# Kernel optimization log

Measured on AMD Instinct MI355X. Metric: run time of the kernel, lower is better.

Reference implementation:

```python
import jax, jax.numpy as jnp
import numpy as np

B, T, H, D = 16, 128, 512, 256
VIN, VOUT = 32000, 32000


def _lstm_cell(xt, h, c, W, U, b):
    # Keras LSTMCell gate order: i, f, g(candidate), o
    z = xt @ W + h @ U + b  # [B, 4H]
    i, f, g, o = jnp.split(z, 4, axis=-1)
    c = jax.nn.sigmoid(f) * c + jax.nn.sigmoid(i) * jnp.tanh(g)
    h = jax.nn.sigmoid(o) * jnp.tanh(c)
    return h, c


def _lstm_seq(x, W, U, b, h0, c0):
    # x: [B,T,Din] -> seq [B,T,H], final (h,c)
    def step(carry, xt):
        h, c = _lstm_cell(xt, carry[0], carry[1], W, U, b)
        return (h, c), h
    (hT, cT), seq = jax.lax.scan(step, (h0, c0), jnp.swapaxes(x, 0, 1))
    return jnp.swapaxes(seq, 0, 1), hT, cT


def setup_inputs() -> dict:
    key = jax.random.key(0)
    ks = jax.random.split(key, 16)
    s = lambda fan: 1.0 / np.sqrt(fan).astype(np.float32)
    f32 = jnp.float32
    return {
        "tokens": jax.random.randint(ks[0], (B, T), 0, VIN + 1),
        "emb": jax.random.normal(ks[1], (VIN + 1, D), f32) * 0.02,
        "W1": jax.random.normal(ks[2], (D, 4 * H), f32) * s(D),
        "U1": jax.random.normal(ks[3], (H, 4 * H), f32) * s(H),
        "b1": jnp.zeros((4 * H,), f32),
        "W2": jax.random.normal(ks[4], (H, 4 * H), f32) * s(H),
        "U2": jax.random.normal(ks[5], (H, 4 * H), f32) * s(H),
        "b2": jnp.zeros((4 * H,), f32),
        "Wd1": jax.random.normal(ks[6], (H, 4 * H), f32) * s(H),
        "Ud1": jax.random.normal(ks[7], (H, 4 * H), f32) * s(H),
        "bd1": jnp.zeros((4 * H,), f32),
        "Wd2": jax.random.normal(ks[8], (H, 4 * H), f32) * s(H),
        "Ud2": jax.random.normal(ks[9], (H, 4 * H), f32) * s(H),
        "bd2": jnp.zeros((4 * H,), f32),
        "Wo": jax.random.normal(ks[10], (2 * H, VOUT + 1), f32) * s(2 * H),
        "bo": jnp.zeros((VOUT + 1,), f32),
    }


def reference(tokens, emb, W1, U1, b1, W2, U2, b2, Wd1, Ud1, bd1, Wd2, Ud2, bd2, Wo, bo):
    x = emb[tokens]  # [B,T,D]
    zeros = jnp.zeros((tokens.shape[0], H), x.dtype)
    seq1, h1, c1 = _lstm_seq(x, W1, U1, b1, zeros, zeros)
    # layer-2 encoder initialized with layer-1 final states (as in source)
    seq2, h2, c2 = _lstm_seq(seq1, W2, U2, b2, h1, c1)

    def dec_step(carry, xt):
        (hA, cA), (hB, cB) = carry
        hA, cA = _lstm_cell(xt, hA, cA, Wd1, Ud1, bd1)
        hB, cB = _lstm_cell(hA, hB, cB, Wd2, Ud2, bd2)
        # global Luong dot attention over full encoder-2 sequence
        score = jax.nn.softmax(jnp.einsum('bsh,bh->bs', seq2, hB), axis=-1)
        ctx = jnp.einsum('bsh,bs->bh', seq2, score)
        out = jnp.concatenate([hB, ctx], axis=-1)  # [B, 2H]
        return ((hA, cA), (hB, cB)), out

    # decoder input is the encoder-2 sequence, time-major
    _, outs = jax.lax.scan(dec_step, ((h1, c1), (h2, c2)), jnp.swapaxes(seq2, 0, 1))
    dec = jnp.swapaxes(outs, 0, 1)  # [B,T,2H]
    logits = dec @ Wo + bo  # [B,T,VOUT+1]
    return jax.nn.softmax(logits, axis=-1)
```

## Files before the change

### kernel.cpp

```cpp
#include <hip/hip_runtime.h>
#include <hip/hip_bf16.h>
#include <math.h>

#define Bq   16
#define Tq   128
#define Hq   512
#define Dq   256
#define G4H  2048
#define MR   2048
#define VO   32001
#define NPAD 32128
#define BH   (Bq * Hq)
#define SENTW 0x7FC0u
#define SENT64 0x7FC07FC07FC07FC0ull
#define NANW 0x7FC00000u
#define SPINCAP (1 << 20)

typedef unsigned int u32;
typedef unsigned long long u64;
typedef __attribute__((ext_vector_type(4))) float f32x4;
typedef __attribute__((ext_vector_type(8))) short bfrag;
typedef __attribute__((ext_vector_type(4))) float facc;

__device__ __forceinline__ float bf2f(short s) {
  union { unsigned u; float f; } v; v.u = ((unsigned)(unsigned short)s) << 16; return v.f;
}
__device__ __forceinline__ short f2bf(float f) {
  union { float f; unsigned u; } v; v.f = f;
  unsigned r = (v.u + 0x7fffu + ((v.u >> 16) & 1u)) >> 16;
  return (short)r;
}
__device__ __forceinline__ float asf(u32 u) {
  union { u32 u; float f; } v; v.u = u; return v.f;
}
__device__ __forceinline__ u32 fbits(float f) {
  union { float f; u32 u; } v; v.f = f; return v.u;
}
__device__ __forceinline__ float sigm(float x) { return 1.0f / (1.0f + expf(-x)); }

__device__ __forceinline__ void ic_store64(u64* p, u64 v) {
  __hip_atomic_store(p, v, __ATOMIC_RELAXED, __HIP_MEMORY_SCOPE_AGENT);
}
__device__ __forceinline__ u64 ic_load64(const u64* p) {
  return __hip_atomic_load(p, __ATOMIC_RELAXED, __HIP_MEMORY_SCOPE_AGENT);
}
__device__ __forceinline__ void ic_store32(u32* p, u32 v) {
  __hip_atomic_store(p, v, __ATOMIC_RELAXED, __HIP_MEMORY_SCOPE_AGENT);
}
__device__ __forceinline__ u32 ic_load32(const u32* p) {
  return __hip_atomic_load(p, __ATOMIC_RELAXED, __HIP_MEMORY_SCOPE_AGENT);
}

__device__ __forceinline__ void* swz(void* plane, int row, int byteoff) {
  return (void*)((char*)plane + row * 1040 + (byteoff ^ ((row & 7) << 4)));
}

__device__ __forceinline__ void stage_h(void* p0, void* p1, const u64 v[8]) {
  #pragma unroll
  for (int it = 0; it < 8; ++it) {
    int i = it * 512 + threadIdx.x;
    int b = i >> 8, bo = (i & 255) * 4;
    *(u32*)swz(p0, b, bo) = (u32)v[it];
    *(u32*)swz(p1, b, bo) = (u32)(v[it] >> 32);
  }
}
__device__ __forceinline__ void stage_x(void* p0, const u32 w[8]) {
  #pragma unroll
  for (int it = 0; it < 8; ++it) {
    int i = it * 512 + threadIdx.x;
    int b = i >> 8, bo = (i & 255) * 4;
    *(u32*)swz(p0, b, bo) = w[it];
  }
}

__global__ __launch_bounds__(256) void k_fill(u64* __restrict__ p, int n) {
  int i = blockIdx.x * 256 + threadIdx.x;
  if (i < n) p[i] = SENT64;
}
__global__ __launch_bounds__(256) void k_fillf(u32* __restrict__ p, int n) {
  int i = blockIdx.x * 256 + threadIdx.x;
  if (i < n) p[i] = NANW;
}

__global__ __launch_bounds__(256) void k_transcvt(const float* __restrict__ in,
                                                  short* __restrict__ out,
                                                  int R, int N, int perm) {
  __shared__ float tile[32][33];
  int nb = blockIdx.x * 32, rb = blockIdx.y * 32;
  int tx = threadIdx.x & 31, ty = threadIdx.x >> 5;
  for (int i = 0; i < 4; ++i) {
    int r = rb + ty + i * 8;
    int n = nb + tx;
    tile[ty + i * 8][tx] = (n < N) ? in[(size_t)r * N + n] : 0.0f;
  }
  __syncthreads();
  for (int i = 0; i < 4; ++i) {
    int n = nb + ty + i * 8;
    int orow = perm ? (((n & 511) << 2) | (n >> 9)) : n;
    out[(size_t)orow * R + rb + tx] = f2bf(tile[tx][ty + i * 8]);
  }
}

__global__ __launch_bounds__(256) void k_gather(const int* __restrict__ tokens,
                                                const float* __restrict__ emb,
                                                short* __restrict__ xbf) {
  int row = blockIdx.x;
  int t = row >> 4, b = row & 15;
  int tok = tokens[b * Tq + t];
  xbf[(size_t)row * Dq + threadIdx.x] = f2bf(emb[(size_t)tok * Dq + threadIdx.x]);
}

__global__ __launch_bounds__(256) void k_gemm(const short* __restrict__ A,
                                              const short* __restrict__ BT,
                                              float* __restrict__ C,
                                              const float* __restrict__ bias,
                                              int M, int Nreal, int K, int ldc,
                                              int permb) {
  __shared__ short lA[128 * 64];
  __shared__ short lB[128 * 64];
  const int tid = threadIdx.x;
  const int wave = tid >> 6, lane = tid & 63;
  const int l15 = lane & 15, l4 = lane >> 4;
  const int m0 = blockIdx.y * 128, n0 = blockIdx.x * 128;
  const int wm = (wave >> 1) * 64, wn = (wave & 1) * 64;
  facc acc[4][4] = {};

  for (int k0 = 0; k0 < K; k0 += 64) {
    __syncthreads();
    for (int i = 0; i < 4; ++i) {
      int c = i * 256 + wave * 64 + lane;
      int r = c >> 3, q = c & 7;
      int qs = q ^ (r & 7);
      const short* ga = A + (size_t)(m0 + r) * K + k0 + qs * 8;
      const short* gb = BT + (size_t)(n0 + r) * K + k0 + qs * 8;
      short* la = lA + (size_t)(i * 256 + wave * 64) * 8;
      short* lb = lB + (size_t)(i * 256 + wave * 64) * 8;
      __builtin_amdgcn_global_load_lds((const __attribute__((address_space(1))) u32*)ga,
                                       (__attribute__((address_space(3))) u32*)la, 16, 0, 0);
      __builtin_amdgcn_global_load_lds((const __attribute__((address_space(1))) u32*)gb,
                                       (__attribute__((address_space(3))) u32*)lb, 16, 0, 0);
    }
    __syncthreads();
    for (int ks = 0; ks < 2; ++ks) {
      bfrag a[4], b[4];
      for (int mi = 0; mi < 4; ++mi) {
        int r = wm + mi * 16 + l15;
        int qs = (ks * 4 + l4) ^ (r & 7);
        a[mi] = *(const bfrag*)&lA[r * 64 + qs * 8];
      }
      for (int ni = 0; ni < 4; ++ni) {
        int r = wn + ni * 16 + l15;
        int qs = (ks * 4 + l4) ^ (r & 7);
        b[ni] = *(const bfrag*)&lB[r * 64 + qs * 8];
      }
      for (int mi = 0; mi < 4; ++mi)
        for (int ni = 0; ni < 4; ++ni)
          acc[mi][ni] = __builtin_amdgcn_mfma_f32_16x16x32_bf16(a[mi], b[ni], acc[mi][ni], 0, 0, 0);
    }
  }
  for (int ni = 0; ni < 4; ++ni) {
    int col = n0 + wn + ni * 16 + l15;
    if (col >= Nreal) continue;
    int bcol = permb ? (((col & 3) << 9) | (col >> 2)) : col;
    float bs = bias ? bias[bcol] : 0.0f;
    for (int mi = 0; mi < 4; ++mi) {
      int rb = m0 + wm + mi * 16 + l4 * 4;
      facc v = acc[mi][ni];
      C[(size_t)(rb + 0) * ldc + col] = v[0] + bs;
      C[(size_t)(rb + 1) * ldc + col] = v[1] + bs;
      C[(size_t)(rb + 2) * ldc + col] = v[2] + bs;
      C[(size_t)(rb + 3) * ldc + col] = v[3] + bs;
    }
  }
}

__global__ __launch_bounds__(512, 1) void k_mega(
    const float* __restrict__ XW,
    const short* __restrict__ U1T, const short* __restrict__ U2T,
    const short* __restrict__ W2T, const short* __restrict__ Ud1T,
    const short* __restrict__ Wd1T, const short* __restrict__ Ud2T,
    const short* __restrict__ Wd2T,
    const float* __restrict__ b2, const float* __restrict__ bd1,
    const float* __restrict__ bd2,
    u64* __restrict__ h1buf, u64* __restrict__ h2buf,
    u64* __restrict__ hAbuf, u64* __restrict__ hBbuf,
    u32* __restrict__ xs1, u32* __restrict__ xs2,
    u32* __restrict__ h1f, u32* __restrict__ c1f,
    u32* __restrict__ h2f, u32* __restrict__ c2f,
    short* __restrict__ seq2_bf, short* __restrict__ hBseq_bf,
    short* __restrict__ dec_bf)
{
  __shared__ short pl[4][16][520];
  __shared__ float zt[8][16][20];
  const int grp  = blockIdx.x >> 5;
  const int rank = blockIdx.x & 31;
  const int tid = threadIdx.x;
  const int wv = tid >> 6, lane = tid & 63;
  const int l15 = lane & 15, l4 = lane >> 4;
  const int kh = wv >> 2;
  const int gw = rank * 4 + (wv & 3);
  const int bb = lane >> 2, jj = lane & 3;
  const int hidx = gw * 4 + jj;
  const int idx = bb * Hq + hidx;
  const int pi = idx >> 1;

  const short* urs = (grp == 0) ? U1T : (grp == 1) ? U2T : (grp == 2) ? Ud1T : Ud2T;
  const short* wrs = (grp == 1) ? W2T : (grp == 2) ? Wd1T : (grp == 3) ? Wd2T : U1T;
  const float* bias = (grp == 1) ? b2 : (grp == 2) ? bd1 : bd2;
  u64* own = (grp == 0) ? h1buf : (grp == 1) ? h2buf : (grp == 2) ? hAbuf : hBbuf;
  const u32* xin = (grp == 1) ? xs1 : xs2;
  u32* xout = (grp == 0) ? xs1 : (grp == 1) ? xs2 : nullptr;

  bfrag ur[8], wr[8];
  {
    size_t ro = (size_t)(gw * 16 + l15) * Hq + kh * 256 + l4 * 8;
    #pragma unroll
    for (int ks = 0; ks < 8; ++ks) {
      ur[ks] = *(const bfrag*)&urs[ro + ks * 32];
      wr[ks] = *(const bfrag*)&wrs[ro + ks * 32];
    }
  }
  float bi = 0, bf_ = 0, bg_ = 0, bo_ = 0;
  if (grp != 0 && wv < 4) {
    bi = bias[hidx]; bf_ = bias[Hq + hidx];
    bg_ = bias[2 * Hq + hidx]; bo_ = bias[3 * Hq + hidx];
  }
  float c = 0.0f;
  if (wv < 4) {
    float hv = 0.0f;
    if (grp != 0) {
      const u32* hf = (grp == 3) ? h2f : h1f;
      const u32* cf = (grp == 3) ? c2f : c1f;
      u32 hw = NANW, cw = NANW;
      for (int spin = 0; spin < SPINCAP; ++spin) {
        hw = ic_load32(&hf[idx]); cw = ic_load32(&cf[idx]);
        if (hw != NANW && cw != NANW) break;
        __builtin_amdgcn_s_sleep(32);
      }
      hv = asf(hw); c = asf(cw);
    }
    int hi_ = (int)(unsigned short)f2bf(hv);
    int lo_ = (int)(unsigned short)f2bf(hv - bf2f((short)hi_));
    int hi2 = __shfl_xor(hi_, 1), lo2 = __shfl_xor(lo_, 1);
    if ((jj & 1) == 0) {
      u64 v = (u64)((u32)hi_ | ((u32)hi2 << 16)) | ((u64)((u32)lo_ | ((u32)lo2 << 16)) << 32);
      ic_store64(&own[pi], v);
    }
  }
  __syncthreads();

  for (int s = 0; s < Tq; ++s) {
    f32x4 xg = {};
    if (grp == 0 && wv < 4)
      xg = *(const f32x4*)&XW[(size_t)(s * Bq + bb) * G4H + hidx * 4];

    u64 v[8], vx[8];
    u32 w[8];
    const u64* ph = own + (size_t)s * 4096 + tid;
    if (grp == 0) {
      for (int spin = 0;; ++spin) {
        #pragma unroll
        for (int it = 0; it < 8; ++it) v[it] = ic_load64(&ph[it * 512]);
        u32 bad = 0;
        #pragma unroll
        for (int it = 0; it < 8; ++it) bad |= (((u32)v[it] & 0xFFFFu) == SENTW);
        if (!bad || spin >= SPINCAP) break;
        __builtin_amdgcn_s_sleep(1);
      }
    } else if (grp != 3) {
      const u32* px = xin + (size_t)s * 4096 + tid;
      for (int spin = 0;; ++spin) {
        #pragma unroll
        for (int it = 0; it < 8; ++it) v[it] = ic_load64(&ph[it * 512]);
        #pragma unroll
        for (int it = 0; it < 8; ++it) w[it] = ic_load32(&px[it * 512]);
        u32 bad = 0;
        #pragma unroll
        for (int it = 0; it < 8; ++it) {
          bad |= (((u32)v[it] & 0xFFFFu) == SENTW);
          bad |= ((w[it] & 0xFFFFu) == SENTW);
        }
        if (!bad || spin >= SPINCAP) break;
        __builtin_amdgcn_s_sleep(1);
      }
    } else {
      const u64* pa = hAbuf + (size_t)(s + 1) * 4096 + tid;
      for (int spin = 0;; ++spin) {
        #pragma unroll
        for (int it = 0; it < 8; ++it) v[it]  = ic_load64(&ph[it * 512]);
        #pragma unroll
        for (int it = 0; it < 8; ++it) vx[it] = ic_load64(&pa[it * 512]);
        u32 bad = 0;
        #pragma unroll
        for (int it = 0; it < 8; ++it) {
          bad |= (((u32)v[it]  & 0xFFFFu) == SENTW);
          bad |= (((u32)vx[it] & 0xFFFFu) == SENTW);
        }
        if (!bad || spin >= SPINCAP) break;
        __builtin_amdgcn_s_sleep(1);
      }
    }
    stage_h(&pl[0][0][0], &pl[1][0][0], v);
    if (grp == 1 || grp == 2) stage_x(&pl[2][0][0], w);
    else if (grp == 3)        stage_h(&pl[2][0][0], &pl[3][0][0], vx);
    __syncthreads();

    facc a0 = {}, a1 = {}, a2 = {}, a3 = {};
    #pragma unroll
    for (int ks = 0; ks < 8; ++ks) {
      int bo = kh * 512 + ks * 64 + l4 * 16;
      bfrag hh = *(const bfrag*)swz(&pl[0][0][0], l15, bo);
      bfrag hl = *(const bfrag*)swz(&pl[1][0][0], l15, bo);
      a0 = __builtin_amdgcn_mfma_f32_16x16x32_bf16(hh, ur[ks], a0, 0, 0, 0);
      a1 = __builtin_amdgcn_mfma_f32_16x16x32_bf16(hl, ur[ks], a1, 0, 0, 0);
      if (grp == 1 || grp == 2) {
        bfrag xh = *(const bfrag*)swz(&pl[2][0][0], l15, bo);
        a2 = __builtin_amdgcn_mfma_f32_16x16x32_bf16(xh, wr[ks], a2, 0, 0, 0);
      } else if (grp == 3) {
        bfrag xh = *(const bfrag*)swz(&pl[2][0][0], l15, bo);
        bfrag xl = *(const bfrag*)swz(&pl[3][0][0], l15, bo);
        a2 = __builtin_amdgcn_mfma_f32_16x16x32_bf16(xh, wr[ks], a2, 0, 0, 0);
        a3 = __builtin_amdgcn_mfma_f32_16x16x32_bf16(xl, wr[ks], a3, 0, 0, 0);
      }
    }
    a0 += a1;
    if (grp != 0) a0 += a2;
    if (grp == 3) a0 += a3;
    *(f32x4*)&zt[wv][l15][l4 * 4] = a0;
    __syncthreads();

    if (wv < 4) {
      float zi = zt[wv][4 * jj + 0][bb] + zt[wv + 4][4 * jj + 0][bb];
      float zf = zt[wv][4 * jj + 1][bb] + zt[wv + 4][4 * jj + 1][bb];
      float zg = zt[wv][4 * jj + 2][bb] + zt[wv + 4][4 * jj + 2][bb];
      float zo = zt[wv][4 * jj + 3][bb] + zt[wv + 4][4 * jj + 3][bb];
      if (grp == 0) { zi += xg[0]; zf += xg[1]; zg += xg[2]; zo += xg[3]; }
      else          { zi += bi;    zf += bf_;   zg += bg_;   zo += bo_;  }
      c = sigm(zf) * c + sigm(zi) * tanhf(zg);
      float hN = sigm(zo) * tanhf(c);
      int hi_ = (int)(unsigned short)f2bf(hN);
      int lo_ = (int)(unsigned short)f2bf(hN - bf2f((short)hi_));
      int hi2 = __shfl_xor(hi_, 1), lo2 = __shfl_xor(lo_, 1);
      if ((jj & 1) == 0) {
        u64 pv = (u64)((u32)hi_ | ((u32)hi2 << 16)) | ((u64)((u32)lo_ | ((u32)lo2 << 16)) << 32);
        ic_store64(&own[(size_t)(s + 1) * 4096 + pi], pv);
        if (xout) ic_store32(&xout[(size_t)s * 4096 + pi], (u32)pv);
      }
      if (grp == 1) seq2_bf[(size_t)(s * Bq + bb) * Hq + hidx] = (short)hi_;
      if (grp == 3) {
        hBseq_bf[(size_t)(s * Bq + bb) * Hq + hidx] = (short)hi_;
        dec_bf[((size_t)bb * Tq + s) * (2 * Hq) + hidx] = (short)hi_;
      }
      if (s == Tq - 1) {
        if (grp == 0) { ic_store32(&h1f[idx], fbits(hN)); ic_store32(&c1f[idx], fbits(c)); }
        if (grp == 1) { ic_store32(&h2f[idx], fbits(hN)); ic_store32(&c2f[idx], fbits(c)); }
      }
    }
  }
}

__global__ __launch_bounds__(256) void k_attn(const short* __restrict__ seq2b,
                                              const short* __restrict__ hqb,
                                              short* __restrict__ decb) {
  int blk = blockIdx.x;
  int b = blk >> 7, t = blk & 127;
  __shared__ u32 q[256];
  __shared__ float part[256];
  __shared__ float p[Tq];
  int tid = threadIdx.x;
  q[tid] = *(const u32*)&hqb[(size_t)(t * Bq + b) * Hq + tid * 2];
  __syncthreads();
  {
    int s = tid >> 1, half = tid & 1;
    const u32* row = (const u32*)&seq2b[(size_t)(s * Bq + b) * Hq + half * 256];
    const u32* qh = q + half * 128;
    float a = 0.0f;
    #pragma unroll 8
    for (int k = 0; k < 128; ++k) {
      u32 r = row[k], qq = qh[k];
      a += asf(r << 16) * asf(qq << 16) + asf(r & 0xFFFF0000u) * asf(qq & 0xFFFF0000u);
    }
    part[tid] = a;
  }
  __syncthreads();
  if (tid < 64) {
    float v0 = part[2 * tid] + part[2 * tid + 1];
    float v1 = part[2 * (tid + 64)] + part[2 * (tid + 64) + 1];
    float mx = fmaxf(v0, v1);
    for (int off = 32; off; off >>= 1) mx = fmaxf(mx, __shfl_xor(mx, off));
    float e0 = __expf(v0 - mx), e1 = __expf(v1 - mx);
    float sm = e0 + e1;
    for (int off = 32; off; off >>= 1) sm += __shfl_xor(sm, off);
    float inv = 1.0f / sm;
    p[tid] = e0 * inv; p[tid + 64] = e1 * inv;
  }
  __syncthreads();
  float c0 = 0.0f, c1 = 0.0f;
  for (int s = 0; s < Tq; ++s) {
    float ps = p[s];
    u32 r = *(const u32*)&seq2b[(size_t)(s * Bq + b) * Hq + tid * 2];
    c0 += ps * asf(r << 16);
    c1 += ps * asf(r & 0xFFFF0000u);
  }
  u32 o = ((u32)(unsigned short)f2bf(c0)) | (((u32)(unsigned short)f2bf(c1)) << 16);
  *(u32*)&decb[(size_t)(b * Tq + t) * (2 * Hq) + Hq + tid * 2] = o;
}

__global__ __launch_bounds__(256) void k_softmax(float* __restrict__ L) {
  int row = blockIdx.x;
  float* p = L + (size_t)row * VO;
  int tid = threadIdx.x;
  float m = -3.0e38f, s = 0.0f;
  for (int i = tid; i < VO; i += 256) {
    float v = p[i];
    float mn = fmaxf(m, v);
    s = s * __expf(m - mn) + __expf(v - mn);
    m = mn;
  }
  __shared__ float sm[256], ss[256];
  sm[tid] = m; ss[tid] = s;
  __syncthreads();
  for (int off = 128; off; off >>= 1) {
    if (tid < off) {
      float m2 = sm[tid + off], s2 = ss[tid + off];
      float mn = fmaxf(sm[tid], m2);
      ss[tid] = ss[tid] * __expf(sm[tid] - mn) + s2 * __expf(m2 - mn);
      sm[tid] = mn;
    }
    __syncthreads();
  }
  float M = sm[0], IS = 1.0f / ss[0];
  for (int i = tid; i < VO; i += 256) {
    p[i] = __expf(p[i] - M) * IS;
  }
}

extern "C" void kernel_launch(void* const* d_in, const int* in_sizes, int n_in,
                              void* d_out, int out_size, void* d_ws, size_t ws_size,
                              hipStream_t stream) {
  const int*   tokens = (const int*)d_in[0];
  const float* emb    = (const float*)d_in[1];
  const float* W1     = (const float*)d_in[2];
  const float* U1     = (const float*)d_in[3];
  const float* b1     = (const float*)d_in[4];
  const float* W2     = (const float*)d_in[5];
  const float* U2     = (const float*)d_in[6];
  const float* b2     = (const float*)d_in[7];
  const float* Wd1    = (const float*)d_in[8];
  const float* Ud1    = (const float*)d_in[9];
  const float* bd1    = (const float*)d_in[10];
  const float* Wd2    = (const float*)d_in[11];
  const float* Ud2    = (const float*)d_in[12];
  const float* bd2    = (const float*)d_in[13];
  const float* Wo     = (const float*)d_in[14];
  const float* bo     = (const float*)d_in[15];
  float* out = (float*)d_out;

  size_t off = 0;
  char* base = (char*)d_ws;
  auto alloc = [&](size_t bytes) -> void* {
    void* p = base + off;
    off += (bytes + 255) & ~(size_t)255;
    return p;
  };
  short* x_bf    = (short*)alloc((size_t)MR * Dq * 2);
  short* W1T     = (short*)alloc((size_t)G4H * Dq * 2);
  short* WoT     = (short*)alloc((size_t)NPAD * (2 * Hq) * 2);
  short* U1T     = (short*)alloc((size_t)G4H * Hq * 2);
  short* U2T     = (short*)alloc((size_t)G4H * Hq * 2);
  short* W2T     = (short*)alloc((size_t)G4H * Hq * 2);
  short* Ud1T    = (short*)alloc((size_t)G4H * Hq * 2);
  short* Wd1T    = (short*)alloc((size_t)G4H * Hq * 2);
  short* Ud2T    = (short*)alloc((size_t)G4H * Hq * 2);
  short* Wd2T    = (short*)alloc((size_t)G4H * Hq * 2);
  float* XW      = (float*)alloc((size_t)MR * G4H * 4);
  short* seq2_bf = (short*)alloc((size_t)MR * Hq * 2);
  short* hBseqbf = (short*)alloc((size_t)MR * Hq * 2);
  short* dec_bf  = (short*)alloc((size_t)MR * 2 * Hq * 2);
  u64*   hflow   = (u64*)alloc((size_t)516 * 4096 * 8);
  u32*   xs1     = (u32*)alloc((size_t)128 * 4096 * 4);
  u32*   xs2     = (u32*)alloc((size_t)128 * 4096 * 4);
  u32*   h1f     = (u32*)alloc(BH * 4);
  u32*   c1f     = (u32*)alloc(BH * 4);
  u32*   h2f     = (u32*)alloc(BH * 4);
  u32*   c2f     = (u32*)alloc(BH * 4);
  u64* h1buf = hflow;
  u64* h2buf = hflow + (size_t)129 * 4096;
  u64* hAbuf = hflow + (size_t)258 * 4096;
  u64* hBbuf = hflow + (size_t)387 * 4096;
  (void)ws_size; (void)in_sizes; (void)n_in; (void)out_size;

  {
    int n64 = 516 * 4096 + 2 * (128 * 4096 / 2);
    k_fill<<<(n64 + 255) / 256, 256, 0, stream>>>(hflow, n64);
    k_fillf<<<(4 * BH + 255) / 256, 256, 0, stream>>>(h1f, 4 * BH);
  }

  k_transcvt<<<dim3(G4H / 32, Dq / 32), 256, 0, stream>>>(W1, W1T, Dq, G4H, 1);
  k_transcvt<<<dim3(G4H / 32, Hq / 32), 256, 0, stream>>>(U1, U1T, Hq, G4H, 1);
  k_transcvt<<<dim3(G4H / 32, Hq / 32), 256, 0, stream>>>(U2, U2T, Hq, G4H, 1);
  k_transcvt<<<dim3(G4H / 32, Hq / 32), 256, 0, stream>>>(W2, W2T, Hq, G4H, 1);
  k_transcvt<<<dim3(G4H / 32, Hq / 32), 256, 0, stream>>>(Ud1, Ud1T, Hq, G4H, 1);
  k_transcvt<<<dim3(G4H / 32, Hq / 32), 256, 0, stream>>>(Wd1, Wd1T, Hq, G4H, 1);
  k_transcvt<<<dim3(G4H / 32, Hq / 32), 256, 0, stream>>>(Ud2, Ud2T, Hq, G4H, 1);
  k_transcvt<<<dim3(G4H / 32, Hq / 32), 256, 0, stream>>>(Wd2, Wd2T, Hq, G4H, 1);
  k_transcvt<<<dim3(NPAD / 32, (2 * Hq) / 32), 256, 0, stream>>>(Wo, WoT, 2 * Hq, VO, 0);

  k_gather<<<MR, 256, 0, stream>>>(tokens, emb, x_bf);

  k_gemm<<<dim3(G4H / 128, MR / 128), 256, 0, stream>>>(x_bf, W1T, XW, b1, MR, G4H, Dq, G4H, 1);

  k_mega<<<128, 512, 0, stream>>>(XW, U1T, U2T, W2T, Ud1T, Wd1T, Ud2T, Wd2T,
                                  b2, bd1, bd2,
                                  h1buf, h2buf, hAbuf, hBbuf, xs1, xs2,
                                  h1f, c1f, h2f, c2f,
                                  seq2_bf, hBseqbf, dec_bf);

  k_attn<<<MR, 256, 0, stream>>>(seq2_bf, hBseqbf, dec_bf);
  k_gemm<<<dim3(NPAD / 128, MR / 128), 256, 0, stream>>>(dec_bf, WoT, out, bo, MR, VO, 2 * Hq, VO, 0);
  k_softmax<<<MR, 256, 0, stream>>>(out);
}
```

Baseline: 2.411 ms.

## Split persistent LSTM megakernel into staged launches with hi/lo input precision

Replaces the single 128-block persistent kernel that ran all four LSTM layers as a wavefront pipeline with three sequential launches: encoder layer 1 alone, then encoder layer 2 together with decoder cell A, then decoder cell B. Final h/c states now cross launch boundaries through plain memory instead of NaN-sentinel spin polls, which removes the extra fill kernel and the bf16 x-stream buffers. Cell inputs are now staged as hi+lo bf16 pairs with two MFMAs, where before only the hi part was used for groups 1 and 2. The cost is the lost overlap between stages, so the four-layer critical path becomes roughly serial, and each step does more MFMA work.

Result: no change. 2.395 ms (-0.7%).

```diff
diff --git a/kernel.cpp b/kernel.cpp
--- a/kernel.cpp
+++ b/kernel.cpp
@@ -13,7 +13,6 @@
 #define BH   (Bq * Hq)
 #define SENTW 0x7FC0u
 #define SENT64 0x7FC07FC07FC07FC0ull
-#define NANW 0x7FC00000u
 #define SPINCAP (1 << 20)
 
 typedef unsigned int u32;
@@ -33,21 +32,12 @@
 __device__ __forceinline__ float asf(u32 u) {
   union { u32 u; float f; } v; v.u = u; return v.f;
 }
-__device__ __forceinline__ u32 fbits(float f) {
-  union { float f; u32 u; } v; v.f = f; return v.u;
-}
 __device__ __forceinline__ float sigm(float x) { return 1.0f / (1.0f + expf(-x)); }
 
 __device__ __forceinline__ void ic_store64(u64* p, u64 v) {
   __hip_atomic_store(p, v, __ATOMIC_RELAXED, __HIP_MEMORY_SCOPE_AGENT);
 }
 __device__ __forceinline__ u64 ic_load64(const u64* p) {
-  return __hip_atomic_load(p, __ATOMIC_RELAXED, __HIP_MEMORY_SCOPE_AGENT);
-}
-__device__ __forceinline__ void ic_store32(u32* p, u32 v) {
-  __hip_atomic_store(p, v, __ATOMIC_RELAXED, __HIP_MEMORY_SCOPE_AGENT);
-}
-__device__ __forceinline__ u32 ic_load32(const u32* p) {
   return __hip_atomic_load(p, __ATOMIC_RELAXED, __HIP_MEMORY_SCOPE_AGENT);
 }
 
@@ -64,22 +54,10 @@
     *(u32*)swz(p1, b, bo) = (u32)(v[it] >> 32);
   }
 }
-__device__ __forceinline__ void stage_x(void* p0, const u32 w[8]) {
-  #pragma unroll
-  for (int it = 0; it < 8; ++it) {
-    int i = it * 512 + threadIdx.x;
-    int b = i >> 8, bo = (i & 255) * 4;
-    *(u32*)swz(p0, b, bo) = w[it];
-  }
-}
 
 __global__ __launch_bounds__(256) void k_fill(u64* __restrict__ p, int n) {
   int i = blockIdx.x * 256 + threadIdx.x;
   if (i < n) p[i] = SENT64;
-}
-__global__ __launch_bounds__(256) void k_fillf(u32* __restrict__ p, int n) {
-  int i = blockIdx.x * 256 + threadIdx.x;
-  if (i < n) p[i] = NANW;
 }
 
 __global__ __launch_bounds__(256) void k_transcvt(const float* __restrict__ in,
@@ -174,26 +152,104 @@
   }
 }
 
-__global__ __launch_bounds__(512, 1) void k_mega(
-    const float* __restrict__ XW,
-    const short* __restrict__ U1T, const short* __restrict__ U2T,
-    const short* __restrict__ W2T, const short* __restrict__ Ud1T,
-    const short* __restrict__ Wd1T, const short* __restrict__ Ud2T,
-    const short* __restrict__ Wd2T,
-    const float* __restrict__ b2, const float* __restrict__ bd1,
-    const float* __restrict__ bd2,
-    u64* __restrict__ h1buf, u64* __restrict__ h2buf,
-    u64* __restrict__ hAbuf, u64* __restrict__ hBbuf,
-    u32* __restrict__ xs1, u32* __restrict__ xs2,
-    u32* __restrict__ h1f, u32* __restrict__ c1f,
-    u32* __restrict__ h2f, u32* __restrict__ c2f,
-    short* __restrict__ seq2_bf, short* __restrict__ hBseq_bf,
-    short* __restrict__ dec_bf)
-{
+
+__global__ __launch_bounds__(512, 1) void k_rec1(const float* __restrict__ XW,
+                                                 const short* __restrict__ UT,
+                                                 u64* __restrict__ hbuf,
+                                                 float* __restrict__ hfin,
+                                                 float* __restrict__ cfin) {
+  __shared__ short lh[2][16][520];
+  __shared__ float zt[8][16][20];
+  const int tid = threadIdx.x;
+  const int wv = tid >> 6, lane = tid & 63;
+  const int l15 = lane & 15, l4 = lane >> 4;
+  const int kh = wv >> 2;
+  const int gw = blockIdx.x * 4 + (wv & 3);
+  const int bb = lane >> 2, jj = lane & 3;
+  const int hidx = gw * 4 + jj;
+
+  bfrag ur[8];
+  {
+    const short* ub = UT + (size_t)(gw * 16 + l15) * Hq + kh * 256 + l4 * 8;
+    #pragma unroll
+    for (int ks = 0; ks < 8; ++ks) ur[ks] = *(const bfrag*)&ub[ks * 32];
+  }
+  float c = 0.0f;
+  if (wv < 4 && (jj & 1) == 0) {
+    ic_store64(&hbuf[(bb * Hq + hidx) >> 1], 0ull);
+  }
+
+  for (int s = 0; s < Tq; ++s) {
+    f32x4 xg = {};
+    if (wv < 4) xg = *(const f32x4*)&XW[(size_t)(s * Bq + bb) * G4H + hidx * 4];
+    const u64* hsrc = hbuf + (size_t)s * 4096 + tid;
+    u64 v[8];
+    for (int spin = 0;; ++spin) {
+      #pragma unroll
+      for (int it = 0; it < 8; ++it) v[it] = ic_load64(&hsrc[it * 512]);
+      u32 bad = 0;
+      #pragma unroll
+      for (int it = 0; it < 8; ++it) bad |= (((u32)v[it] & 0xFFFFu) == SENTW);
+      if (!bad || spin >= SPINCAP) break;
+      __builtin_amdgcn_s_sleep(1);
+    }
+    stage_h(&lh[0][0][0], &lh[1][0][0], v);
+    __syncthreads();
+    facc a0 = {}, a1 = {};
+    #pragma unroll
+    for (int ks = 0; ks < 8; ++ks) {
+      int bo = kh * 512 + ks * 64 + l4 * 16;
+      bfrag ah = *(const bfrag*)swz(&lh[0][0][0], l15, bo);
+      bfrag al = *(const bfrag*)swz(&lh[1][0][0], l15, bo);
+      a0 = __builtin_amdgcn_mfma_f32_16x16x32_bf16(ah, ur[ks], a0, 0, 0, 0);
+      a1 = __builtin_amdgcn_mfma_f32_16x16x32_bf16(al, ur[ks], a1, 0, 0, 0);
+    }
+    a0 += a1;
+    *(f32x4*)&zt[wv][l15][l4 * 4] = a0;
+    __syncthreads();
+    if (wv < 4) {
+      float zi = zt[wv][4 * jj + 0][bb] + zt[wv + 4][4 * jj + 0][bb] + xg[0];
+      float zf = zt[wv][4 * jj + 1][bb] + zt[wv + 4][4 * jj + 1][bb] + xg[1];
+      float zg = zt[wv][4 * jj + 2][bb] + zt[wv + 4][4 * jj + 2][bb] + xg[2];
+      float zo = zt[wv][4 * jj + 3][bb] + zt[wv + 4][4 * jj + 3][bb] + xg[3];
+      c = sigm(zf) * c + sigm(zi) * tanhf(zg);
+      float hN = sigm(zo) * tanhf(c);
+      int hi_ = (int)(unsigned short)f2bf(hN);
+      int lo_ = (int)(unsigned short)f2bf(hN - bf2f((short)hi_));
+      int hi2 = __shfl_xor(hi_, 1), lo2 = __shfl_xor(lo_, 1);
+      if ((jj & 1) == 0) {
+        u64 pv = (u64)((u32)hi_ | ((u32)hi2 << 16)) | ((u64)((u32)lo_ | ((u32)lo2 << 16)) << 32);
+        ic_store64(&hbuf[(size_t)(s + 1) * 4096 + ((bb * Hq + hidx) >> 1)], pv);
+      }
+      if (s == Tq - 1) {
+        hfin[bb * Hq + hidx] = hN;
+        cfin[bb * Hq + hidx] = c;
+      }
+    }
+  }
+}
+
+struct CellP {
+  const short* ur;
+  const short* wr;
+  const float* bias;
+  const float* hcar;
+  const float* ccar;
+  u64*  own;
+  const u64* inp;
+  int   inpPoll;
+  short* seq;
+  short* dec;
+  float* hfin;
+  float* cfin;
+};
+struct Params2 { CellP c[2]; };
+
+__global__ __launch_bounds__(512, 1) void k_cells(Params2 prm) {
   __shared__ short pl[4][16][520];
   __shared__ float zt[8][16][20];
-  const int grp  = blockIdx.x >> 5;
-  const int rank = blockIdx.x & 31;
+  const int grp = blockIdx.x >> 5, rank = blockIdx.x & 31;
+  const CellP P = grp ? prm.c[1] : prm.c[0];
   const int tid = threadIdx.x;
   const int wv = tid >> 6, lane = tid & 63;
   const int l15 = lane & 15, l4 = lane >> 4;
@@ -202,62 +258,53 @@
   const int bb = lane >> 2, jj = lane & 3;
   const int hidx = gw * 4 + jj;
   const int idx = bb * Hq + hidx;
-  const int pi = idx >> 1;
-
-  const short* urs = (grp == 0) ? U1T : (grp == 1) ? U2T : (grp == 2) ? Ud1T : Ud2T;
-  const short* wrs = (grp == 1) ? W2T : (grp == 2) ? Wd1T : (grp == 3) ? Wd2T : U1T;
-  const float* bias = (grp == 1) ? b2 : (grp == 2) ? bd1 : bd2;
-  u64* own = (grp == 0) ? h1buf : (grp == 1) ? h2buf : (grp == 2) ? hAbuf : hBbuf;
-  const u32* xin = (grp == 1) ? xs1 : xs2;
-  u32* xout = (grp == 0) ? xs1 : (grp == 1) ? xs2 : nullptr;
 
   bfrag ur[8], wr[8];
   {
     size_t ro = (size_t)(gw * 16 + l15) * Hq + kh * 256 + l4 * 8;
     #pragma unroll
     for (int ks = 0; ks < 8; ++ks) {
-      ur[ks] = *(const bfrag*)&urs[ro + ks * 32];
-      wr[ks] = *(const bfrag*)&wrs[ro + ks * 32];
-    }
-  }
-  float bi = 0, bf_ = 0, bg_ = 0, bo_ = 0;
-  if (grp != 0 && wv < 4) {
-    bi = bias[hidx]; bf_ = bias[Hq + hidx];
-    bg_ = bias[2 * Hq + hidx]; bo_ = bias[3 * Hq + hidx];
-  }
-  float c = 0.0f;
+      ur[ks] = *(const bfrag*)&P.ur[ro + ks * 32];
+      wr[ks] = *(const bfrag*)&P.wr[ro + ks * 32];
+    }
+  }
+  float bi = 0, bf_ = 0, bg_ = 0, bo_ = 0, c = 0.0f;
   if (wv < 4) {
-    float hv = 0.0f;
-    if (grp != 0) {
-      const u32* hf = (grp == 3) ? h2f : h1f;
-      const u32* cf = (grp == 3) ? c2f : c1f;
-      u32 hw = NANW, cw = NANW;
-      for (int spin = 0; spin < SPINCAP; ++spin) {
-        hw = ic_load32(&hf[idx]); cw = ic_load32(&cf[idx]);
-        if (hw != NANW && cw != NANW) break;
-        __builtin_amdgcn_s_sleep(32);
-      }
-      hv = asf(hw); c = asf(cw);
-    }
+    bi = P.bias[hidx]; bf_ = P.bias[Hq + hidx];
+    bg_ = P.bias[2 * Hq + hidx]; bo_ = P.bias[3 * Hq + hidx];
+    float hv = P.hcar[idx];
+    c = P.ccar[idx];
     int hi_ = (int)(unsigned short)f2bf(hv);
     int lo_ = (int)(unsigned short)f2bf(hv - bf2f((short)hi_));
     int hi2 = __shfl_xor(hi_, 1), lo2 = __shfl_xor(lo_, 1);
     if ((jj & 1) == 0) {
       u64 v = (u64)((u32)hi_ | ((u32)hi2 << 16)) | ((u64)((u32)lo_ | ((u32)lo2 << 16)) << 32);
-      ic_store64(&own[pi], v);
-    }
-  }
-  __syncthreads();
+      ic_store64(&P.own[idx >> 1], v);
+    }
+  }
 
   for (int s = 0; s < Tq; ++s) {
-    f32x4 xg = {};
-    if (grp == 0 && wv < 4)
-      xg = *(const f32x4*)&XW[(size_t)(s * Bq + bb) * G4H + hidx * 4];
-
     u64 v[8], vx[8];
-    u32 w[8];
-    const u64* ph = own + (size_t)s * 4096 + tid;
-    if (grp == 0) {
+    const u64* ph = P.own + (size_t)s * 4096 + tid;
+    const u64* px = P.inp + (size_t)(s + 1) * 4096 + tid;
+    if (P.inpPoll) {
+      for (int spin = 0;; ++spin) {
+        #pragma unroll
+        for (int it = 0; it < 8; ++it) v[it]  = ic_load64(&ph[it * 512]);
+        #pragma unroll
+        for (int it = 0; it < 8; ++it) vx[it] = ic_load64(&px[it * 512]);
+        u32 bad = 0;
+        #pragma unroll
+        for (int it = 0; it < 8; ++it) {
+          bad |= (((u32)v[it]  & 0xFFFFu) == SENTW);
+          bad |= (((u32)vx[it] & 0xFFFFu) == SENTW);
+        }
+        if (!bad || spin >= SPINCAP) break;
+        __builtin_amdgcn_s_sleep(1);
+      }
+    } else {
+      #pragma unroll
+      for (int it = 0; it < 8; ++it) vx[it] = px[it * 512];
       for (int spin = 0;; ++spin) {
         #pragma unroll
         for (int it = 0; it < 8; ++it) v[it] = ic_load64(&ph[it * 512]);
@@ -267,42 +314,9 @@
         if (!bad || spin >= SPINCAP) break;
         __builtin_amdgcn_s_sleep(1);
       }
-    } else if (grp != 3) {
-      const u32* px = xin + (size_t)s * 4096 + tid;
-      for (int spin = 0;; ++spin) {
-        #pragma unroll
-        for (int it = 0; it < 8; ++it) v[it] = ic_load64(&ph[it * 512]);
-        #pragma unroll
-        for (int it = 0; it < 8; ++it) w[it] = ic_load32(&px[it * 512]);
-        u32 bad = 0;
-        #pragma unroll
-        for (int it = 0; it < 8; ++it) {
-          bad |= (((u32)v[it] & 0xFFFFu) == SENTW);
-          bad |= ((w[it] & 0xFFFFu) == SENTW);
-        }
-        if (!bad || spin >= SPINCAP) break;
-        __builtin_amdgcn_s_sleep(1);
-      }
-    } else {
-      const u64* pa = hAbuf + (size_t)(s + 1) * 4096 + tid;
-      for (int spin = 0;; ++spin) {
-        #pragma unroll
-        for (int it = 0; it < 8; ++it) v[it]  = ic_load64(&ph[it * 512]);
-        #pragma unroll
-        for (int it = 0; it < 8; ++it) vx[it] = ic_load64(&pa[it * 512]);
-        u32 bad = 0;
-        #pragma unroll
-        for (int it = 0; it < 8; ++it) {
-          bad |= (((u32)v[it]  & 0xFFFFu) == SENTW);
-          bad |= (((u32)vx[it] & 0xFFFFu) == SENTW);
-        }
-        if (!bad || spin >= SPINCAP) break;
-        __builtin_amdgcn_s_sleep(1);
-      }
     }
     stage_h(&pl[0][0][0], &pl[1][0][0], v);
-    if (grp == 1 || grp == 2) stage_x(&pl[2][0][0], w);
-    else if (grp == 3)        stage_h(&pl[2][0][0], &pl[3][0][0], vx);
+    stage_h(&pl[2][0][0], &pl[3][0][0], vx);
     __syncthreads();
 
     facc a0 = {}, a1 = {}, a2 = {}, a3 = {};
@@ -311,31 +325,22 @@
       int bo = kh * 512 + ks * 64 + l4 * 16;
       bfrag hh = *(const bfrag*)swz(&pl[0][0][0], l15, bo);
       bfrag hl = *(const bfrag*)swz(&pl[1][0][0], l15, bo);
+      bfrag xh = *(const bfrag*)swz(&pl[2][0][0], l15, bo);
+      bfrag xl = *(const bfrag*)swz(&pl[3][0][0], l15, bo);
       a0 = __builtin_amdgcn_mfma_f32_16x16x32_bf16(hh, ur[ks], a0, 0, 0, 0);
       a1 = __builtin_amdgcn_mfma_f32_16x16x32_bf16(hl, ur[ks], a1, 0, 0, 0);
-      if (grp == 1 || grp == 2) {
-        bfrag xh = *(const bfrag*)swz(&pl[2][0][0], l15, bo);
-        a2 = __builtin_amdgcn_mfma_f32_16x16x32_bf16(xh, wr[ks], a2, 0, 0, 0);
-      } else if (grp == 3) {
-        bfrag xh = *(const bfrag*)swz(&pl[2][0][0], l15, bo);
-        bfrag xl = *(const bfrag*)swz(&pl[3][0][0], l15, bo);
-        a2 = __builtin_amdgcn_mfma_f32_16x16x32_bf16(xh, wr[ks], a2, 0, 0, 0);
-        a3 = __builtin_amdgcn_mfma_f32_16x16x32_bf16(xl, wr[ks], a3, 0, 0, 0);
-      }
-    }
-    a0 += a1;
-    if (grp != 0) a0 += a2;
-    if (grp == 3) a0 += a3;
+      a2 = __builtin_amdgcn_mfma_f32_16x16x32_bf16(xh, wr[ks], a2, 0, 0, 0);
+      a3 = __builtin_amdgcn_mfma_f32_16x16x32_bf16(xl, wr[ks], a3, 0, 0, 0);
+    }
+    a0 += a1; a0 += a2; a0 += a3;
     *(f32x4*)&zt[wv][l15][l4 * 4] = a0;
     __syncthreads();
 
     if (wv < 4) {
-      float zi = zt[wv][4 * jj + 0][bb] + zt[wv + 4][4 * jj + 0][bb];
-      float zf = zt[wv][4 * jj + 1][bb] + zt[wv + 4][4 * jj + 1][bb];
-      float zg = zt[wv][4 * jj + 2][bb] + zt[wv + 4][4 * jj + 2][bb];
-      float zo = zt[wv][4 * jj + 3][bb] + zt[wv + 4][4 * jj + 3][bb];
-      if (grp == 0) { zi += xg[0]; zf += xg[1]; zg += xg[2]; zo += xg[3]; }
-      else          { zi += bi;    zf += bf_;   zg += bg_;   zo += bo_;  }
+      float zi = zt[wv][4 * jj + 0][bb] + zt[wv + 4][4 * jj + 0][bb] + bi;
+      float zf = zt[wv][4 * jj + 1][bb] + zt[wv + 4][4 * jj + 1][bb] + bf_;
+      float zg = zt[wv][4 * jj + 2][bb] + zt[wv + 4][4 * jj + 2][bb] + bg_;
+      float zo = zt[wv][4 * jj + 3][bb] + zt[wv + 4][4 * jj + 3][bb] + bo_;
       c = sigm(zf) * c + sigm(zi) * tanhf(zg);
       float hN = sigm(zo) * tanhf(c);
       int hi_ = (int)(unsigned short)f2bf(hN);
@@ -343,17 +348,13 @@
       int hi2 = __shfl_xor(hi_, 1), lo2 = __shfl_xor(lo_, 1);
       if ((jj & 1) == 0) {
         u64 pv = (u64)((u32)hi_ | ((u32)hi2 << 16)) | ((u64)((u32)lo_ | ((u32)lo2 << 16)) << 32);
-        ic_store64(&own[(size_t)(s + 1) * 4096 + pi], pv);
-        if (xout) ic_store32(&xout[(size_t)s * 4096 + pi], (u32)pv);
-      }
-      if (grp == 1) seq2_bf[(size_t)(s * Bq + bb) * Hq + hidx] = (short)hi_;
-      if (grp == 3) {
-        hBseq_bf[(size_t)(s * Bq + bb) * Hq + hidx] = (short)hi_;
-        dec_bf[((size_t)bb * Tq + s) * (2 * Hq) + hidx] = (short)hi_;
-      }
-      if (s == Tq - 1) {
-        if (grp == 0) { ic_store32(&h1f[idx], fbits(hN)); ic_store32(&c1f[idx], fbits(c)); }
-        if (grp == 1) { ic_store32(&h2f[idx], fbits(hN)); ic_store32(&c2f[idx], fbits(c)); }
+        ic_store64(&P.own[(size_t)(s + 1) * 4096 + (idx >> 1)], pv);
+      }
+      if (P.seq) P.seq[(size_t)(s * Bq + bb) * Hq + hidx] = (short)hi_;
+      if (P.dec) P.dec[((size_t)bb * Tq + s) * (2 * Hq) + hidx] = (short)hi_;
+      if (s == Tq - 1 && P.hfin) {
+        P.hfin[idx] = hN;
+        P.cfin[idx] = c;
       }
     }
   }
@@ -478,12 +479,10 @@
   short* hBseqbf = (short*)alloc((size_t)MR * Hq * 2);
   short* dec_bf  = (short*)alloc((size_t)MR * 2 * Hq * 2);
   u64*   hflow   = (u64*)alloc((size_t)516 * 4096 * 8);
-  u32*   xs1     = (u32*)alloc((size_t)128 * 4096 * 4);
-  u32*   xs2     = (u32*)alloc((size_t)128 * 4096 * 4);
-  u32*   h1f     = (u32*)alloc(BH * 4);
-  u32*   c1f     = (u32*)alloc(BH * 4);
-  u32*   h2f     = (u32*)alloc(BH * 4);
-  u32*   c2f     = (u32*)alloc(BH * 4);
+  float* h1f     = (float*)alloc(BH * 4);
+  float* c1f     = (float*)alloc(BH * 4);
+  float* h2f     = (float*)alloc(BH * 4);
+  float* c2f     = (float*)alloc(BH * 4);
   u64* h1buf = hflow;
   u64* h2buf = hflow + (size_t)129 * 4096;
   u64* hAbuf = hflow + (size_t)258 * 4096;
@@ -491,9 +490,8 @@
   (void)ws_size; (void)in_sizes; (void)n_in; (void)out_size;
 
   {
-    int n64 = 516 * 4096 + 2 * (128 * 4096 / 2);
+    int n64 = 516 * 4096;
     k_fill<<<(n64 + 255) / 256, 256, 0, stream>>>(hflow, n64);
-    k_fillf<<<(4 * BH + 255) / 256, 256, 0, stream>>>(h1f, 4 * BH);
   }
 
   k_transcvt<<<dim3(G4H / 32, Dq / 32), 256, 0, stream>>>(W1, W1T, Dq, G4H, 1);
@@ -509,12 +507,21 @@
   k_gather<<<MR, 256, 0, stream>>>(tokens, emb, x_bf);
 
   k_gemm<<<dim3(G4H / 128, MR / 128), 256, 0, stream>>>(x_bf, W1T, XW, b1, MR, G4H, Dq, G4H, 1);
-
-  k_mega<<<128, 512, 0, stream>>>(XW, U1T, U2T, W2T, Ud1T, Wd1T, Ud2T, Wd2T,
-                                  b2, bd1, bd2,
-                                  h1buf, h2buf, hAbuf, hBbuf, xs1, xs2,
-                                  h1f, c1f, h2f, c2f,
-                                  seq2_bf, hBseqbf, dec_bf);
+  k_rec1<<<32, 512, 0, stream>>>(XW, U1T, h1buf, h1f, c1f);
+
+  {
+    Params2 p;
+    p.c[0] = { U2T, W2T, b2,  h1f, c1f, h2buf, h1buf, 0, seq2_bf, nullptr, h2f, c2f };
+    p.c[1] = { Ud1T, Wd1T, bd1, h1f, c1f, hAbuf, h2buf, 1, nullptr, nullptr, nullptr, nullptr };
+    k_cells<<<64, 512, 0, stream>>>(p);
+  }
+
+  {
+    Params2 p;
+    p.c[0] = { Ud2T, Wd2T, bd2, h2f, c2f, hBbuf, hAbuf, 0, hBseqbf, dec_bf, nullptr, nullptr };
+    p.c[1] = p.c[0];
+    k_cells<<<32, 512, 0, stream>>>(p);
+  }
 
   k_attn<<<MR, 256, 0, stream>>>(seq2_bf, hBseqbf, dec_bf);
   k_gemm<<<dim3(NPAD / 128, MR / 128), 256, 0, stream>>>(dec_bf, WoT, out, bo, MR, VO, 2 * Hq, VO, 0);
```
